# Optimization experiments

Hardware: AMD Instinct MI355X
Metric: run time of the kernel (lower is better)

## Reference

```python
import jax, jax.numpy as jnp
import numpy as np


def _grid_sample_3d(x, grid):
    """Trilinear 3D grid_sample, align_corners=False, zero padding.
    x: [B,C,D,H,W]; grid: [B,D,H,W,3] with (gx,gy,gz) in [-1,1] indexing (W,H,D).
    """
    B, C, D, H, W = x.shape
    gx, gy, gz = grid[..., 0], grid[..., 1], grid[..., 2]
    # unnormalize (align_corners=False)
    ix = ((gx + 1.0) * W - 1.0) * 0.5
    iy = ((gy + 1.0) * H - 1.0) * 0.5
    iz = ((gz + 1.0) * D - 1.0) * 0.5
    ix0f = jnp.floor(ix); iy0f = jnp.floor(iy); iz0f = jnp.floor(iz)
    fx = ix - ix0f; fy = iy - iy0f; fz = iz - iz0f
    ix0 = ix0f.astype(jnp.int32); iy0 = iy0f.astype(jnp.int32); iz0 = iz0f.astype(jnp.int32)
    N = D * H * W
    x_flat = x.reshape(B, C, N)
    out = jnp.zeros_like(x)
    for dz in (0, 1):
        for dy in (0, 1):
            for dx in (0, 1):
                xi = ix0 + dx; yi = iy0 + dy; zi = iz0 + dz
                w = ((fx if dx else 1.0 - fx)
                     * (fy if dy else 1.0 - fy)
                     * (fz if dz else 1.0 - fz))
                valid = ((xi >= 0) & (xi < W) & (yi >= 0) & (yi < H)
                         & (zi >= 0) & (zi < D))
                xc = jnp.clip(xi, 0, W - 1)
                yc = jnp.clip(yi, 0, H - 1)
                zc = jnp.clip(zi, 0, D - 1)
                idx = (zc * H + yc) * W + xc  # [B,D,H,W]
                g = jnp.take_along_axis(x_flat, idx.reshape(B, 1, N), axis=2)
                g = g.reshape(B, C, D, H, W)
                out = out + g * (w * valid)[:, None]
    return out


def setup_inputs() -> dict:
    key = jax.random.key(0)
    k1, k2, k3, k4 = jax.random.split(key, 4)
    B, C, D, H, W = 8, 4, 128, 128, 128
    F_DIM = 512
    x = jax.random.normal(k1, (B, C, D, H, W), dtype=jnp.float32)
    im_feat = jax.random.normal(k2, (B, F_DIM), dtype=jnp.float32)
    pos_w = jax.random.normal(k3, (2, F_DIM), dtype=jnp.float32) * 0.02
    pos_b = jax.random.normal(k4, (2,), dtype=jnp.float32) * 0.02
    return {"x": x, "im_feat": im_feat, "pos_w": pos_w, "pos_b": pos_b}


def reference(x, im_feat, pos_w, pos_b):
    B, C, D, H, W = x.shape
    mu_rho = im_feat @ pos_w.T + pos_b  # [B,2]
    mu, rho = mu_rho[:, 0], mu_rho[:, 1]
    cm, sm = jnp.cos(mu), jnp.sin(mu)
    cr, sr = jnp.cos(rho), jnp.sin(rho)
    zero = jnp.zeros_like(mu); one = jnp.ones_like(mu)
    # rotation about x-axis by rho, about y-axis by mu: [B,3,3]
    rot_x = jnp.stack([
        jnp.stack([one, zero, zero], -1),
        jnp.stack([zero, cr, sr], -1),
        jnp.stack([zero, -sr, cr], -1)], -2)
    rot_y = jnp.stack([
        jnp.stack([cm, zero, -sm], -1),
        jnp.stack([zero, one, zero], -1),
        jnp.stack([sm, zero, cm], -1)], -2)
    R = jnp.einsum('bij,bjk->bik', rot_y, rot_x)
    X = jnp.linspace(-1.0, 1.0, W, dtype=x.dtype)
    Y = jnp.linspace(-1.0, 1.0, H, dtype=x.dtype)
    Z = jnp.linspace(-1.0, 1.0, D, dtype=x.dtype)
    zz, yy, xx = jnp.meshgrid(Z, Y, X, indexing='ij')  # [D,H,W]
    coords = jnp.stack([xx, yy, zz], -1)               # [D,H,W,3]
    grid = jnp.einsum('bij,dhwj->bdhwi', R, coords)    # [B,D,H,W,3]
    return _grid_sample_3d(x, grid)
```

## Files before the change

kernel.cpp:

```cpp
#include <hip/hip_runtime.h>
#include <hip/hip_fp16.h>

#define DHW (128*128*128)

typedef unsigned int u32x4 __attribute__((ext_vector_type(4)));

__global__ void compute_R_kernel(const float* __restrict__ im_feat,
                                 const float* __restrict__ pos_w,
                                 const float* __restrict__ pos_b,
                                 float* __restrict__ Rout) {
    int b = blockIdx.x;
    int t = threadIdx.x;
    const float* f = im_feat + b * 512;
    float s0 = 0.f, s1 = 0.f;
    for (int i = t; i < 512; i += 64) {
        float v = f[i];
        s0 = fmaf(v, pos_w[i], s0);
        s1 = fmaf(v, pos_w[512 + i], s1);
    }
    for (int off = 32; off > 0; off >>= 1) {
        s0 += __shfl_down(s0, off, 64);
        s1 += __shfl_down(s1, off, 64);
    }
    if (t == 0) {
        float mu  = s0 + pos_b[0];
        float rho = s1 + pos_b[1];
        float cm = cosf(mu),  sm = sinf(mu);
        float cr = cosf(rho), sr = sinf(rho);
        float* R = Rout + b * 16;
        R[0] = cm;   R[1] = sm * sr;  R[2] = -sm * cr;
        R[3] = 0.f;  R[4] = cr;       R[5] = sr;
        R[6] = sm;   R[7] = -cm * sr; R[8] = cm * cr;
    }
}

__global__ __launch_bounds__(256) void transpose_pack_kernel(const float* __restrict__ x,
                                                             uint2* __restrict__ xt) {
    unsigned tid = blockIdx.x * 256u + threadIdx.x;
    unsigned spatial = tid & (DHW - 1u);
    unsigned b = tid >> 21;
    const float* xb = x + (size_t)(b << 2) * DHW + spatial;
    float a0 = xb[0];
    float a1 = xb[DHW];
    float a2 = xb[2u * DHW];
    float a3 = xb[3u * DHW];
    unsigned lo = (unsigned)__half_as_ushort(__float2half_rn(a0)) |
                  ((unsigned)__half_as_ushort(__float2half_rn(a1)) << 16);
    unsigned hi = (unsigned)__half_as_ushort(__float2half_rn(a2)) |
                  ((unsigned)__half_as_ushort(__float2half_rn(a3)) << 16);
    xt[(size_t)tid] = make_uint2(lo, hi);
}

__device__ inline float2 up2(unsigned u) {
    __half2 h = reinterpret_cast<const __half2&>(u);
    return __half22float2(h);
}

__global__ __launch_bounds__(256) void sample_kernel_h(const char* __restrict__ xt,
                                                       const float* __restrict__ Rin,
                                                       float* __restrict__ out) {
    unsigned bid = blockIdx.x;
    int b = (int)(bid >> 13);
    unsigned spatial = ((bid & 8191u) << 8) | threadIdx.x;

    int w = spatial & 127;
    int h = (spatial >> 7) & 127;
    int d = spatial >> 14;
    h = __builtin_amdgcn_readfirstlane(h);
    d = __builtin_amdgcn_readfirstlane(d);

    const float* R = Rin + b * 16;
    const float step = 2.0f / 127.0f;
    float X = fmaf((float)w, step, -1.0f);
    float Y = fmaf((float)h, step, -1.0f);
    float Z = fmaf((float)d, step, -1.0f);

    float gx = fmaf(R[0], X, fmaf(R[1], Y, R[2] * Z));
    float gy = fmaf(R[4], Y, R[5] * Z);
    float gz = fmaf(R[6], X, fmaf(R[7], Y, R[8] * Z));

    float ix = fmaf(gx, 64.0f, 63.5f);
    float iy = fmaf(gy, 64.0f, 63.5f);
    float iz = fmaf(gz, 64.0f, 63.5f);

    float fx0 = floorf(ix), fy0 = floorf(iy), fz0 = floorf(iz);
    float fx = ix - fx0, fy = iy - fy0, fz = iz - fz0;
    int ix0 = (int)fx0, iy0 = (int)fy0, iz0 = (int)fz0;
    int ix1 = ix0 + 1, iy1 = iy0 + 1, iz1 = iz0 + 1;

    float wx0 = ((unsigned)ix0 < 128u) ? (1.f - fx) : 0.f;
    float wx1 = ((unsigned)ix1 < 128u) ? fx : 0.f;
    float wy0 = ((unsigned)iy0 < 128u) ? (1.f - fy) : 0.f;
    float wy1 = ((unsigned)iy1 < 128u) ? fy : 0.f;
    float wz0 = ((unsigned)iz0 < 128u) ? (1.f - fz) : 0.f;
    float wz1 = ((unsigned)iz1 < 128u) ? fz : 0.f;

    float* ob = out + (size_t)(b << 2) * DHW + spatial;

    if ((wx0 + wx1) * (wy0 + wy1) * (wz0 + wz1) == 0.f) {
        __builtin_nontemporal_store(0.f, ob);
        __builtin_nontemporal_store(0.f, ob + DHW);
        __builtin_nontemporal_store(0.f, ob + 2 * DHW);
        __builtin_nontemporal_store(0.f, ob + 3 * DHW);
        return;
    }

    int yc0 = min(max(iy0, 0), 127), yc1 = min(max(iy1, 0), 127);
    int zc0 = min(max(iz0, 0), 127), zc1 = min(max(iz1, 0), 127);

    int base = min(max(ix0, 0), 126);
    float sw0 = (base == ix0 ? wx0 : 0.f) + (base == ix1 ? wx1 : 0.f);
    float sw1 = (base + 1 == ix0 ? wx0 : 0.f) + (base + 1 == ix1 ? wx1 : 0.f);

    const char* xb = xt + (size_t)b * (DHW * 8);
    unsigned o00 = (((unsigned)(zc0 * 128 + yc0) << 7) + (unsigned)base) << 3;
    unsigned o01 = (((unsigned)(zc0 * 128 + yc1) << 7) + (unsigned)base) << 3;
    unsigned o10 = (((unsigned)(zc1 * 128 + yc0) << 7) + (unsigned)base) << 3;
    unsigned o11 = (((unsigned)(zc1 * 128 + yc1) << 7) + (unsigned)base) << 3;

    u32x4 q0, q1, q2, q3;
    asm volatile("global_load_dwordx4 %0, %1, off" : "=v"(q0) : "v"(xb + o00));
    asm volatile("global_load_dwordx4 %0, %1, off" : "=v"(q1) : "v"(xb + o01));
    asm volatile("global_load_dwordx4 %0, %1, off" : "=v"(q2) : "v"(xb + o10));
    asm volatile("global_load_dwordx4 %0, %1, off" : "=v"(q3) : "v"(xb + o11));
    asm volatile("s_waitcnt vmcnt(0)" ::: "memory");
    __builtin_amdgcn_sched_barrier(0);

    float w00 = wz0 * wy0, w01 = wz0 * wy1, w10 = wz1 * wy0, w11 = wz1 * wy1;

    float a0 = 0.f, a1 = 0.f, a2 = 0.f, a3 = 0.f;
    {
        float ws0 = sw0 * w00, ws1 = sw1 * w00;
        float2 p0 = up2(q0.x), p1 = up2(q0.y), p2 = up2(q0.z), p3 = up2(q0.w);
        a0 = fmaf(p0.x, ws0, fmaf(p2.x, ws1, a0));
        a1 = fmaf(p0.y, ws0, fmaf(p2.y, ws1, a1));
        a2 = fmaf(p1.x, ws0, fmaf(p3.x, ws1, a2));
        a3 = fmaf(p1.y, ws0, fmaf(p3.y, ws1, a3));
    }
    {
        float ws0 = sw0 * w01, ws1 = sw1 * w01;
        float2 p0 = up2(q1.x), p1 = up2(q1.y), p2 = up2(q1.z), p3 = up2(q1.w);
        a0 = fmaf(p0.x, ws0, fmaf(p2.x, ws1, a0));
        a1 = fmaf(p0.y, ws0, fmaf(p2.y, ws1, a1));
        a2 = fmaf(p1.x, ws0, fmaf(p3.x, ws1, a2));
        a3 = fmaf(p1.y, ws0, fmaf(p3.y, ws1, a3));
    }
    {
        float ws0 = sw0 * w10, ws1 = sw1 * w10;
        float2 p0 = up2(q2.x), p1 = up2(q2.y), p2 = up2(q2.z), p3 = up2(q2.w);
        a0 = fmaf(p0.x, ws0, fmaf(p2.x, ws1, a0));
        a1 = fmaf(p0.y, ws0, fmaf(p2.y, ws1, a1));
        a2 = fmaf(p1.x, ws0, fmaf(p3.x, ws1, a2));
        a3 = fmaf(p1.y, ws0, fmaf(p3.y, ws1, a3));
    }
    {
        float ws0 = sw0 * w11, ws1 = sw1 * w11;
        float2 p0 = up2(q3.x), p1 = up2(q3.y), p2 = up2(q3.z), p3 = up2(q3.w);
        a0 = fmaf(p0.x, ws0, fmaf(p2.x, ws1, a0));
        a1 = fmaf(p0.y, ws0, fmaf(p2.y, ws1, a1));
        a2 = fmaf(p1.x, ws0, fmaf(p3.x, ws1, a2));
        a3 = fmaf(p1.y, ws0, fmaf(p3.y, ws1, a3));
    }

    __builtin_nontemporal_store(a0, ob);
    __builtin_nontemporal_store(a1, ob + DHW);
    __builtin_nontemporal_store(a2, ob + 2 * DHW);
    __builtin_nontemporal_store(a3, ob + 3 * DHW);
}

__global__ __launch_bounds__(256) void sample_kernel(const float* __restrict__ x,
                                                     const float* __restrict__ Rin,
                                                     float* __restrict__ out) {
    unsigned bid = blockIdx.x;
    int b = (int)(bid >> 13);
    unsigned spatial = ((bid & 8191u) << 8) | threadIdx.x;

    int w = spatial & 127;
    int h = (spatial >> 7) & 127;
    int d = spatial >> 14;

    const float* R = Rin + b * 16;
    const float step = 2.0f / 127.0f;
    float X = fmaf((float)w, step, -1.0f);
    float Y = fmaf((float)h, step, -1.0f);
    float Z = fmaf((float)d, step, -1.0f);

    float gx = fmaf(R[0], X, fmaf(R[1], Y, R[2] * Z));
    float gy = fmaf(R[4], Y, R[5] * Z);
    float gz = fmaf(R[6], X, fmaf(R[7], Y, R[8] * Z));

    float ix = fmaf(gx, 64.0f, 63.5f);
    float iy = fmaf(gy, 64.0f, 63.5f);
    float iz = fmaf(gz, 64.0f, 63.5f);

    float fx0 = floorf(ix), fy0 = floorf(iy), fz0 = floorf(iz);
    float fx = ix - fx0, fy = iy - fy0, fz = iz - fz0;
    int ix0 = (int)fx0, iy0 = (int)fy0, iz0 = (int)fz0;
    int ix1 = ix0 + 1, iy1 = iy0 + 1, iz1 = iz0 + 1;

    float wx0 = ((unsigned)ix0 < 128u) ? (1.f - fx) : 0.f;
    float wx1 = ((unsigned)ix1 < 128u) ? fx : 0.f;
    float wy0 = ((unsigned)iy0 < 128u) ? (1.f - fy) : 0.f;
    float wy1 = ((unsigned)iy1 < 128u) ? fy : 0.f;
    float wz0 = ((unsigned)iz0 < 128u) ? (1.f - fz) : 0.f;
    float wz1 = ((unsigned)iz1 < 128u) ? fz : 0.f;

    float* ob = out + (size_t)(b << 2) * DHW + spatial;

    if ((wx0 + wx1) * (wy0 + wy1) * (wz0 + wz1) == 0.f) {
        __builtin_nontemporal_store(0.f, ob);
        __builtin_nontemporal_store(0.f, ob + DHW);
        __builtin_nontemporal_store(0.f, ob + 2 * DHW);
        __builtin_nontemporal_store(0.f, ob + 3 * DHW);
        return;
    }

    int xc0 = min(max(ix0, 0), 127), xc1 = min(max(ix1, 0), 127);
    int yc0 = min(max(iy0, 0), 127), yc1 = min(max(iy1, 0), 127);
    int zc0 = min(max(iz0, 0), 127), zc1 = min(max(iz1, 0), 127);

    int r00 = (zc0 * 128 + yc0) * 128;
    int r01 = (zc0 * 128 + yc1) * 128;
    int r10 = (zc1 * 128 + yc0) * 128;
    int r11 = (zc1 * 128 + yc1) * 128;

    int o0 = r00 + xc0, o1 = r00 + xc1;
    int o2 = r01 + xc0, o3 = r01 + xc1;
    int o4 = r10 + xc0, o5 = r10 + xc1;
    int o6 = r11 + xc0, o7 = r11 + xc1;

    const float* xb = x + (size_t)(b << 2) * DHW;

    float v[4][8];
#pragma unroll
    for (int c = 0; c < 4; ++c) {
        const float* xc = xb + (size_t)c * DHW;
        v[c][0] = xc[o0]; v[c][1] = xc[o1];
        v[c][2] = xc[o2]; v[c][3] = xc[o3];
        v[c][4] = xc[o4]; v[c][5] = xc[o5];
        v[c][6] = xc[o6]; v[c][7] = xc[o7];
    }

    float w00 = wz0 * wy0, w01 = wz0 * wy1, w10 = wz1 * wy0, w11 = wz1 * wy1;

#pragma unroll
    for (int c = 0; c < 4; ++c) {
        float acc;
        acc  = (v[c][0] * wx0 + v[c][1] * wx1) * w00;
        acc += (v[c][2] * wx0 + v[c][3] * wx1) * w01;
        acc += (v[c][4] * wx0 + v[c][5] * wx1) * w10;
        acc += (v[c][6] * wx0 + v[c][7] * wx1) * w11;
        __builtin_nontemporal_store(acc, ob + (size_t)c * DHW);
    }
}

extern "C" void kernel_launch(void* const* d_in, const int* in_sizes, int n_in,
                              void* d_out, int out_size, void* d_ws, size_t ws_size,
                              hipStream_t stream) {
    const float* x       = (const float*)d_in[0];
    const float* im_feat = (const float*)d_in[1];
    const float* pos_w   = (const float*)d_in[2];
    const float* pos_b   = (const float*)d_in[3];
    float* out = (float*)d_out;

    float* Rws = (float*)d_ws;
    const size_t XT_OFF = 1024;
    size_t need = XT_OFF + (size_t)8 * DHW * 8 + 64;

    compute_R_kernel<<<8, 64, 0, stream>>>(im_feat, pos_w, pos_b, Rws);

    int total = 8 * DHW;
    if (ws_size >= need) {
        uint2* xt = (uint2*)((char*)d_ws + XT_OFF);
        transpose_pack_kernel<<<total / 256, 256, 0, stream>>>(x, xt);
        sample_kernel_h<<<total / 256, 256, 0, stream>>>((const char*)xt, Rws, out);
    } else {
        sample_kernel<<<total / 256, 256, 0, stream>>>(x, Rws, out);
    }
}
```

Baseline: 536.6 us.

## Vectorize pack kernel and remap sample threads to 32x2 tiles with XCD swizzle

The pack kernel now has each thread read float2 pairs and write one uint4 holding two spatial points of packed fp16 channels, halving the thread count and widening memory transactions. The sample kernel remaps each wavefront to cover 32 w by 2 d instead of 64 w in a row, giving the rotated gather a more compact 2D footprint. It also interleaves block IDs across the 8 batches so consecutive blocks land on different batches, presumably to spread work across XCDs and their L2 caches. The cost is that d is no longer wave-uniform, and output stores become two 128-byte segments per wave instead of one contiguous 256-byte run.

```diff
diff --git a/kernel.cpp b/kernel.cpp
--- a/kernel.cpp
+++ b/kernel.cpp
@@ -35,20 +35,25 @@
 }
 
 __global__ __launch_bounds__(256) void transpose_pack_kernel(const float* __restrict__ x,
-                                                             uint2* __restrict__ xt) {
-    unsigned tid = blockIdx.x * 256u + threadIdx.x;
-    unsigned spatial = tid & (DHW - 1u);
-    unsigned b = tid >> 21;
-    const float* xb = x + (size_t)(b << 2) * DHW + spatial;
-    float a0 = xb[0];
-    float a1 = xb[DHW];
-    float a2 = xb[2u * DHW];
-    float a3 = xb[3u * DHW];
-    unsigned lo = (unsigned)__half_as_ushort(__float2half_rn(a0)) |
-                  ((unsigned)__half_as_ushort(__float2half_rn(a1)) << 16);
-    unsigned hi = (unsigned)__half_as_ushort(__float2half_rn(a2)) |
-                  ((unsigned)__half_as_ushort(__float2half_rn(a3)) << 16);
-    xt[(size_t)tid] = make_uint2(lo, hi);
+                                                             uint4* __restrict__ xt) {
+    unsigned t = blockIdx.x * 256u + threadIdx.x;
+    unsigned sp2 = t & (DHW / 2 - 1u);
+    unsigned b = t >> 20;
+    const float2* xb = (const float2*)x + (size_t)(b << 2) * (DHW / 2) + sp2;
+    float2 a0 = xb[0];
+    float2 a1 = xb[DHW / 2];
+    float2 a2 = xb[2 * (DHW / 2)];
+    float2 a3 = xb[3 * (DHW / 2)];
+    uint4 o;
+    o.x = (unsigned)__half_as_ushort(__float2half_rn(a0.x)) |
+          ((unsigned)__half_as_ushort(__float2half_rn(a1.x)) << 16);
+    o.y = (unsigned)__half_as_ushort(__float2half_rn(a2.x)) |
+          ((unsigned)__half_as_ushort(__float2half_rn(a3.x)) << 16);
+    o.z = (unsigned)__half_as_ushort(__float2half_rn(a0.y)) |
+          ((unsigned)__half_as_ushort(__float2half_rn(a1.y)) << 16);
+    o.w = (unsigned)__half_as_ushort(__float2half_rn(a2.y)) |
+          ((unsigned)__half_as_ushort(__float2half_rn(a3.y)) << 16);
+    xt[(size_t)b * (DHW / 2) + sp2] = o;
 }
 
 __device__ inline float2 up2(unsigned u) {
@@ -60,14 +65,14 @@
                                                        const float* __restrict__ Rin,
                                                        float* __restrict__ out) {
     unsigned bid = blockIdx.x;
-    int b = (int)(bid >> 13);
-    unsigned spatial = ((bid & 8191u) << 8) | threadIdx.x;
-
-    int w = spatial & 127;
-    int h = (spatial >> 7) & 127;
-    int d = spatial >> 14;
+    unsigned wg = ((bid & 7u) << 13) | (bid >> 3);
+    int b = (int)(wg >> 13);
+    unsigned lane = threadIdx.x & 63u;
+    unsigned i2 = (wg << 2) | (threadIdx.x >> 6);
+    int w = (int)(((i2 & 3u) << 5) | (lane & 31u));
+    int h = (int)((i2 >> 2) & 127u);
+    int d = (int)((((i2 >> 9) & 63u) << 1) | (lane >> 5));
     h = __builtin_amdgcn_readfirstlane(h);
-    d = __builtin_amdgcn_readfirstlane(d);
 
     const float* R = Rin + b * 16;
     const float step = 2.0f / 127.0f;
@@ -95,6 +100,7 @@
     float wz0 = ((unsigned)iz0 < 128u) ? (1.f - fz) : 0.f;
     float wz1 = ((unsigned)iz1 < 128u) ? fz : 0.f;
 
+    unsigned spatial = (((unsigned)(d * 128 + h)) << 7) | (unsigned)w;
     float* ob = out + (size_t)(b << 2) * DHW + spatial;
 
     if ((wx0 + wx1) * (wy0 + wy1) * (wz0 + wz1) == 0.f) {
@@ -271,8 +277,8 @@
 
     int total = 8 * DHW;
     if (ws_size >= need) {
-        uint2* xt = (uint2*)((char*)d_ws + XT_OFF);
-        transpose_pack_kernel<<<total / 256, 256, 0, stream>>>(x, xt);
+        uint4* xt = (uint4*)((char*)d_ws + XT_OFF);
+        transpose_pack_kernel<<<total / 512, 256, 0, stream>>>(x, xt);
         sample_kernel_h<<<total / 256, 256, 0, stream>>>((const char*)xt, Rws, out);
     } else {
         sample_kernel<<<total / 256, 256, 0, stream>>>(x, Rws, out);
```

Result: slower. 589.8 us (+9.9%).
